# Kernel tuning notes

Hardware: AMD Instinct MI355X
Metric: run time of the kernel (lower is better)

Reference implementation:

```python
import jax, jax.numpy as jnp
import numpy as np
from jax import lax

H, W = 4096, 4096

def setup_inputs() -> dict:
    key = jax.random.key(0)
    k_occ, k_seed = jax.random.split(key)
    occupied = (jax.random.uniform(k_occ, (H, W)) < 0.3).astype(jnp.float32)
    flood = ((jax.random.uniform(k_seed, (H, W)) < 1e-3).astype(jnp.float32)
             * (1.0 - occupied))
    flood_input = jnp.stack([occupied, flood], axis=-1)  # [H, W, 2]
    flood_count = jnp.zeros((H, W), dtype=jnp.float32)
    # Fixed flood kernel, HWIO layout: (3, 3, in=2, out=1)
    kernel = jnp.zeros((3, 3, 2, 1), dtype=jnp.float32)
    kernel = kernel.at[1, 1, 0, 0].set(-5.0)  # occupied center blocks flood
    kernel = kernel.at[1, 2, 1, 0].set(1.0)   # right
    kernel = kernel.at[2, 1, 1, 0].set(1.0)   # down
    kernel = kernel.at[1, 0, 1, 0].set(1.0)   # left
    kernel = kernel.at[0, 1, 1, 0].set(1.0)   # up
    kernel = kernel.at[1, 1, 1, 0].set(1.0)   # center
    bias = jnp.zeros((1,), dtype=jnp.float32)
    return {"flood_input": flood_input, "flood_count": flood_count,
            "kernel": kernel, "bias": bias, "num_steps": 16}

def reference(flood_input, flood_count, kernel, bias, num_steps):
    dn = ("NHWC", "HWIO", "NHWC")

    def flood_step(carry, _):
        x, count = carry                      # x: [H, W, 2], count: [H, W]
        occupied = x[..., 0]
        y = lax.conv_general_dilated(x[None], kernel, (1, 1), "SAME",
                                     dimension_numbers=dn)[0, ..., 0] + bias[0]
        y = jnp.clip(y, 0.0, 1.0)             # flooded frontier
        new_x = jnp.stack([occupied, y], axis=-1)
        return (new_x, count + y), None

    (x_final, count_final), _ = lax.scan(flood_step,
                                         (flood_input, flood_count),
                                         None, length=num_steps)
    # [H, W, 3]: occupied, flood, count
    return jnp.concatenate([x_final, count_final[..., None]], axis=-1)
```

## Files before the change

kernel.cpp:

```cpp
#include <hip/hip_runtime.h>


typedef unsigned long long u64;
typedef float f32x4 __attribute__((ext_vector_type(4)));
typedef float f32x2 __attribute__((ext_vector_type(2)));

#define HH 4096
#define WW 4096
#define WPR 64
#define NSTEPS 16
#define HALO 16
#define IT 32

__global__ __launch_bounds__(256) void pack_kernel(
    const float* __restrict__ flood_input,
    u64* __restrict__ occP, u64* __restrict__ flP)
{
    const int lane = threadIdx.x & 63;
    const int wv   = threadIdx.x >> 6;
    const int r    = blockIdx.x;
#pragma unroll
    for (int b = 0; b < 2; ++b) {
        float vx[8], vy[8];
#pragma unroll
        for (int j = 0; j < 8; ++j) {
            const int w = wv * 16 + b * 8 + j;
            const f32x2 v = __builtin_nontemporal_load(
                (const f32x2*)(flood_input +
                                ((size_t)r * WW + (w << 6) + lane) * 2));
            vx[j] = v[0]; vy[j] = v[1];
        }
#pragma unroll
        for (int j = 0; j < 8; ++j) {
            const int w = wv * 16 + b * 8 + j;
            const u64 om = __ballot(vx[j] > 0.5f);
            const u64 fm = __ballot(vy[j] > 0.5f);
            if (lane == 0) {
                occP[(size_t)r * WPR + w] = om;
                flP [(size_t)r * WPR + w] = fm;
            }
        }
    }
}

__global__ __launch_bounds__(256, 8) void flood_kernel(
    const u64* __restrict__ occP, const u64* __restrict__ flP,
    const float* __restrict__ flood_count,
    float* __restrict__ out)
{
    __shared__ u64 plane[4][IT][7];
    __shared__ float out2[4][7 * 104 + 96];

    const int tid  = threadIdx.x;
    const int lane = tid & 63;
    const int wv   = tid >> 6;

    const int tile_r0 = blockIdx.y * IT;
    const int tile_c0 = blockIdx.x * (4 * IT) + wv * IT;

    const int gr  = tile_r0 - HALO + lane;
    const bool rin = (gr >= 0) & (gr < HH);
    const int s   = tile_c0 - HALO;
    const int q0  = ((s + 64) >> 6) - 1;
    const int sh  = s - (q0 << 6);

    const size_t base = (size_t)(rin ? gr : 0) * WPR;
    const int qa = min(max(q0, 0), WPR - 1);
    const int qb = min(max(q0 + 1, 0), WPR - 1);
    u64 o0 = occP[base + qa], o1 = occP[base + qb];
    u64 f0 = flP [base + qa], f1 = flP [base + qb];
    const bool va = rin & (q0 >= 0);
    const bool vb = rin & (q0 + 1 < WPR);
    if (!va) { o0 = ~0ull; f0 = 0ull; }
    if (!vb) { o1 = ~0ull; f1 = 0ull; }
    const u64 occ = (o0 >> sh) | (sh ? (o1 << (64 - sh)) : 0ull);
    u64       f   = (f0 >> sh) | (sh ? (f1 << (64 - sh)) : 0ull);

    const int rsub = lane >> 3;
    const int g    = lane & 7;
    const float* fcbase = flood_count + (size_t)(tile_r0 + rsub) * WW
                          + tile_c0 + g * 4;
    f32x4 fc_next = __builtin_nontemporal_load((const f32x4*)fcbase);

    const u64 nocc = ~occ;
    u64 c0 = 0, c1 = 0, c2 = 0, c3 = 0, c4 = 0;
#pragma unroll
    for (int it = 0; it < NSTEPS; ++it) {
        u64 up = __shfl_up(f, 1);
        u64 dn = __shfl_down(f, 1);
        if (lane == 0)  up = 0ull;
        if (lane == 63) dn = 0ull;
        f = nocc & (f | (f << 1) | (f >> 1) | up | dn);
        u64 c = f, t;
        t = c0; c0 = t ^ c; c = t & c;
        t = c1; c1 = t ^ c; c = t & c;
        t = c2; c2 = t ^ c; c = t & c;
        t = c3; c3 = t ^ c; c = t & c;
        c4 ^= c;
    }

    if (lane >= HALO && lane < HALO + IT) {
        u64* p = plane[wv][lane - HALO];
        p[0] = occ; p[1] = f;
        p[2] = c0; p[3] = c1; p[4] = c2; p[5] = c3; p[6] = c4;
    }
    asm volatile("s_waitcnt lgkmcnt(0)" ::: "memory");

    const int bit0 = HALO + g * 4;
    for (int t = 0; t < 4; ++t) {
        const f32x4 fc4 = fc_next;
        if (t + 1 < 4)
            fc_next = __builtin_nontemporal_load(
                (const f32x4*)(fcbase + (size_t)(t + 1) * 8 * WW));

        const int irow = t * 8 + rsub;
        const u64* p = plane[wv][irow];
        const u64 ow = p[0], fw = p[1];
        const u64 k0 = p[2], k1 = p[3], k2 = p[4], k3 = p[5], k4 = p[6];

        float v[12];
#pragma unroll
        for (int j = 0; j < 4; ++j) {
            const int bit = bit0 + j;
            int cv = (int)((k0 >> bit) & 1ull)
                   + ((int)((k1 >> bit) & 1ull) << 1)
                   + ((int)((k2 >> bit) & 1ull) << 2)
                   + ((int)((k3 >> bit) & 1ull) << 3)
                   + ((int)((k4 >> bit) & 1ull) << 4);
            v[j*3+0] = (float)((ow >> bit) & 1ull);
            v[j*3+1] = (float)((fw >> bit) & 1ull);
            v[j*3+2] = (float)cv + fc4[j];
        }
        float* dst = &out2[wv][rsub * 104 + g * 12];
        *(f32x4*)(dst + 0) = (f32x4){v[0], v[1], v[2],  v[3]};
        *(f32x4*)(dst + 4) = (f32x4){v[4], v[5], v[6],  v[7]};
        *(f32x4*)(dst + 8) = (f32x4){v[8], v[9], v[10], v[11]};

        asm volatile("s_waitcnt lgkmcnt(0)" ::: "memory");

#pragma unroll
        for (int st = 0; st < 3; ++st) {
            const int L   = st * 256 + lane * 4;
            const int row = L / 96;
            const int off = L - row * 96;
            const f32x4 q = *(const f32x4*)(&out2[wv][row * 104 + off]);
            __builtin_nontemporal_store(q,
                (f32x4*)(out + ((size_t)(tile_r0 + t * 8 + row) * WW
                                + tile_c0) * 3 + off));
        }
    }
}

extern "C" void kernel_launch(void* const* d_in, const int* in_sizes, int n_in,
                              void* d_out, int out_size, void* d_ws, size_t ws_size,
                              hipStream_t stream) {
    const float* flood_input = (const float*)d_in[0];
    const float* flood_cnt   = (const float*)d_in[1];
    float* out = (float*)d_out;

    u64* occP = (u64*)d_ws;
    u64* flP  = occP + (size_t)HH * WPR;

    pack_kernel<<<dim3(HH), dim3(256), 0, stream>>>(flood_input, occP, flP);

    dim3 grid(WW / (4 * IT), HH / IT);
    flood_kernel<<<grid, dim3(256), 0, stream>>>(occP, flP, flood_cnt, out);
}
```

Measured before the change: 371.2 us.

## Remap output epilogue so each wave writes full 128-column block rows

The epilogue now has each wave handle whole rows spanning all four 32-column sub-tiles of the block, instead of its own 32-column tile. Output stores and flood_count loads therefore become longer contiguous runs (384 floats per row rather than 96), which should give better-coalesced global traffic. Because waves now read bit-planes written by other waves, a block-wide __syncthreads replaces the wave-local LDS wait, adding a barrier.

```diff
diff --git a/kernel.cpp b/kernel.cpp
--- a/kernel.cpp
+++ b/kernel.cpp
@@ -49,7 +49,7 @@
     float* __restrict__ out)
 {
     __shared__ u64 plane[4][IT][7];
-    __shared__ float out2[4][7 * 104 + 96];
+    __shared__ float out2[4][2 * 128 * 3];
 
     const int tid  = threadIdx.x;
     const int lane = tid & 63;
@@ -57,6 +57,7 @@
 
     const int tile_r0 = blockIdx.y * IT;
     const int tile_c0 = blockIdx.x * (4 * IT) + wv * IT;
+    const int bc0     = blockIdx.x * (4 * IT);
 
     const int gr  = tile_r0 - HALO + lane;
     const bool rin = (gr >= 0) & (gr < HH);
@@ -76,10 +77,11 @@
     const u64 occ = (o0 >> sh) | (sh ? (o1 << (64 - sh)) : 0ull);
     u64       f   = (f0 >> sh) | (sh ? (f1 << (64 - sh)) : 0ull);
 
-    const int rsub = lane >> 3;
-    const int g    = lane & 7;
-    const float* fcbase = flood_count + (size_t)(tile_r0 + rsub) * WW
-                          + tile_c0 + g * 4;
+    const int half = lane >> 5;
+    const int l32  = lane & 31;
+    const int col0 = l32 * 4;
+    const float* fcbase = flood_count +
+        (size_t)(tile_r0 + wv * 8 + half) * WW + bc0 + col0;
     f32x4 fc_next = __builtin_nontemporal_load((const f32x4*)fcbase);
 
     const u64 nocc = ~occ;
@@ -104,17 +106,19 @@
         p[0] = occ; p[1] = f;
         p[2] = c0; p[3] = c1; p[4] = c2; p[5] = c3; p[6] = c4;
     }
-    asm volatile("s_waitcnt lgkmcnt(0)" ::: "memory");
+    __syncthreads();
 
-    const int bit0 = HALO + g * 4;
+    const int sw   = col0 >> 5;
+    const int bit0 = HALO + (col0 & 31);
     for (int t = 0; t < 4; ++t) {
         const f32x4 fc4 = fc_next;
         if (t + 1 < 4)
             fc_next = __builtin_nontemporal_load(
-                (const f32x4*)(fcbase + (size_t)(t + 1) * 8 * WW));
+                (const f32x4*)(fcbase + (size_t)(t + 1) * 2 * WW));
 
-        const int irow = t * 8 + rsub;
-        const u64* p = plane[wv][irow];
+        const int rA   = wv * 8 + 2 * t;
+        const int irow = rA + half;
+        const u64* p = plane[sw][irow];
         const u64 ow = p[0], fw = p[1];
         const u64 k0 = p[2], k1 = p[3], k2 = p[4], k3 = p[5], k4 = p[6];
 
@@ -131,7 +135,7 @@
             v[j*3+1] = (float)((fw >> bit) & 1ull);
             v[j*3+2] = (float)cv + fc4[j];
         }
-        float* dst = &out2[wv][rsub * 104 + g * 12];
+        float* dst = &out2[wv][half * 384 + l32 * 12];
         *(f32x4*)(dst + 0) = (f32x4){v[0], v[1], v[2],  v[3]};
         *(f32x4*)(dst + 4) = (f32x4){v[4], v[5], v[6],  v[7]};
         *(f32x4*)(dst + 8) = (f32x4){v[8], v[9], v[10], v[11]};
@@ -141,12 +145,12 @@
 #pragma unroll
         for (int st = 0; st < 3; ++st) {
             const int L   = st * 256 + lane * 4;
-            const int row = L / 96;
-            const int off = L - row * 96;
-            const f32x4 q = *(const f32x4*)(&out2[wv][row * 104 + off]);
+            const int row = (L >= 384) ? 1 : 0;
+            const int off = L - row * 384;
+            const f32x4 q = *(const f32x4*)(&out2[wv][L]);
             __builtin_nontemporal_store(q,
-                (f32x4*)(out + ((size_t)(tile_r0 + t * 8 + row) * WW
-                                + tile_c0) * 3 + off));
+                (f32x4*)(out + ((size_t)(tile_r0 + rA + row) * WW + bc0) * 3
+                         + off));
         }
     }
 }
```

After: 366.9 us. No clear change (-1.1%).
